# Kernel tuning notes

Measured on AMD Instinct MI355X. Metric: run time of the kernel, lower is better.

## Reference

```python
import jax, jax.numpy as jnp
import numpy as np

DIM = 768
HEADS = 12
HEAD_DIM = DIM // HEADS
SCALE = HEAD_DIM ** -0.5


def setup_inputs() -> dict:
    key = jax.random.key(0)
    k1, k2, k3, k4, k5 = jax.random.split(key, 5)
    B, N, C = 8, 1024, DIM
    x = jax.random.normal(k1, (B, N, C), dtype=jnp.float32)
    scale_emb = jax.random.normal(k2, (1, 1, C), dtype=jnp.float32)
    # nn.Linear weights stored as (out, in); bias only on proj
    w_qkv = jax.random.normal(k3, (3 * C, C), dtype=jnp.float32) * (C ** -0.5)
    w_proj = jax.random.normal(k4, (C, C), dtype=jnp.float32) * (C ** -0.5)
    b_proj = jax.random.normal(k5, (C,), dtype=jnp.float32) * 0.01
    return {"x": x, "scale_emb": scale_emb, "w_qkv": w_qkv, "w_proj": w_proj, "b_proj": b_proj}


def reference(x, scale_emb, w_qkv, w_proj, b_proj):
    B, N, C = x.shape
    H, D = HEADS, HEAD_DIM
    # qkv: (B, N, 3C) -> (3, B, H, N, D)
    qkv = jnp.einsum('bnc,oc->bno', x, w_qkv)
    qkv = qkv.reshape(B, N, 3, H, D).transpose(2, 0, 3, 1, 4)
    q, k, v = qkv[0], qkv[1], qkv[2]
    # scale_emb broadcast to (B, H, N, D) and added to k
    se = jnp.broadcast_to(scale_emb, (B, N, C)).reshape(B, N, H, D).transpose(0, 2, 1, 3)
    k = k + se
    attn_logits = jnp.einsum('bhnd,bhmd->bhnm', q, k) * SCALE
    attn_probs = jax.nn.softmax(attn_logits, axis=-1)
    out = jnp.einsum('bhnm,bhmd->bhnd', attn_probs, v)
    out = out.transpose(0, 2, 1, 3).reshape(B, N, C)
    out = jnp.einsum('bnc,oc->bno', out, w_proj) + b_proj
    return out, attn_probs
```

## Files before the change

kernel.cpp:

```cpp
#include <hip/hip_runtime.h>
#include <hip/hip_bf16.h>


typedef unsigned short u16;
typedef __attribute__((ext_vector_type(8))) short bf16x8;
typedef __attribute__((ext_vector_type(4))) float f32x4;

#define DEVI static __device__ __forceinline__

DEVI u16 f2bf(float f) {
  union { float f; unsigned int u; } v; v.f = f;
  return (u16)((v.u + 0x7fffu + ((v.u >> 16) & 1u)) >> 16);
}

DEVI void gload16(const void* g, void* l) {
  __builtin_amdgcn_global_load_lds(
      (const __attribute__((address_space(1))) unsigned int*)g,
      (__attribute__((address_space(3))) unsigned int*)l, 16, 0, 0);
}

__global__ void cvt_f32_bf16(const float* __restrict__ src, u16* __restrict__ dst, int n4) {
  int i = blockIdx.x * 256 + threadIdx.x;
  if (i >= n4) return;
  float4 f = ((const float4*)src)[i];
  unsigned int lo = f2bf(f.x) | ((unsigned int)f2bf(f.y) << 16);
  unsigned int hi = f2bf(f.z) | ((unsigned int)f2bf(f.w) << 16);
  ((uint2*)dst)[i] = make_uint2(lo, hi);
}

template<int MODE>
__global__ __launch_bounds__(256)
void gemm128(const u16* __restrict__ A, const u16* __restrict__ Bw, int K,
             const float* __restrict__ se,
             u16* __restrict__ qo, u16* __restrict__ ko, u16* __restrict__ vto,
             const float* __restrict__ bias, float* __restrict__ out)
{
  __shared__ u16 lA[128 * 32];
  __shared__ u16 lB[128 * 32];
  const int mt = blockIdx.x, nt = blockIdx.y;
  const int t = threadIdx.x;
  const int w = t >> 6, l = t & 63, lhi = l >> 4, llo = l & 15;
  const int wr = w >> 1, wc = w & 1;

  f32x4 acc[4][4];
#pragma unroll
  for (int m = 0; m < 4; ++m)
#pragma unroll
    for (int n = 0; n < 4; ++n) acc[m][n] = f32x4{0.f, 0.f, 0.f, 0.f};

  const size_t arow0 = (size_t)mt * 128, brow0 = (size_t)nt * 128;

  for (int k0 = 0; k0 < K; k0 += 32) {
#pragma unroll
    for (int r = 0; r < 2; ++r) {
      int idx = r * 256 + t;
      int row = idx >> 2, col = (idx & 3) * 8;
      gload16(A + (arow0 + row) * K + k0 + col, &lA[idx * 8]);
      gload16(Bw + (brow0 + row) * K + k0 + col, &lB[idx * 8]);
    }
    __syncthreads();
    bf16x8 af[4], bfr[4];
#pragma unroll
    for (int m = 0; m < 4; ++m)
      af[m] = *(const bf16x8*)&lA[(wr * 64 + m * 16 + llo) * 32 + lhi * 8];
#pragma unroll
    for (int n = 0; n < 4; ++n)
      bfr[n] = *(const bf16x8*)&lB[(wc * 64 + n * 16 + llo) * 32 + lhi * 8];
#pragma unroll
    for (int m = 0; m < 4; ++m)
#pragma unroll
      for (int n = 0; n < 4; ++n)
        acc[m][n] = __builtin_amdgcn_mfma_f32_16x16x32_bf16(af[m], bfr[n], acc[m][n], 0, 0, 0);
    __syncthreads();
  }

  if (MODE == 0) {
    const int part = nt / 6;
#pragma unroll
    for (int n = 0; n < 4; ++n) {
      const int gcol = (int)brow0 + wc * 64 + n * 16 + llo;
      const int c = gcol - part * 768;
      const int h = c >> 6, d = c & 63;
      const float sev = (part == 1) ? se[c] : 0.f;
#pragma unroll
      for (int m = 0; m < 4; ++m) {
#pragma unroll
        for (int j = 0; j < 4; ++j) {
          const int tok = (int)arow0 + wr * 64 + m * 16 + lhi * 4 + j;
          const int b = tok >> 10, ntok = tok & 1023;
          const size_t bhh = (size_t)(b * 12 + h);
          const float v = acc[m][n][j];
          if (part == 0)      qo[(bhh * 1024 + ntok) * 64 + d] = f2bf(v * 0.125f);
          else if (part == 1) ko[(bhh * 1024 + ntok) * 64 + d] = f2bf(v + sev);
          else                vto[(bhh * 64 + d) * 1024 + ntok] = f2bf(v);
        }
      }
    }
  } else {
#pragma unroll
    for (int m = 0; m < 4; ++m)
#pragma unroll
      for (int j = 0; j < 4; ++j) {
        const int tok = (int)arow0 + wr * 64 + m * 16 + lhi * 4 + j;
#pragma unroll
        for (int n = 0; n < 4; ++n) {
          const int gcol = (int)brow0 + wc * 64 + n * 16 + llo;
          out[(size_t)tok * 768 + gcol] = acc[m][n][j] + bias[gcol];
        }
      }
  }
}

__global__ __launch_bounds__(256)
void attn_fused(const u16* __restrict__ q, const u16* __restrict__ kin,
                const u16* __restrict__ vt, float* __restrict__ probs,
                u16* __restrict__ ao)
{
  __shared__ u16 lq[32 * 64];
  __shared__ u16 lk[256 * 64];
  __shared__ u16 lp[32 * 264];
  __shared__ float red[4][32];
  const int qt = blockIdx.x, bh = blockIdx.y;
  const int t = threadIdx.x;
  const int w = t >> 6, l = t & 63, lhi = l >> 4, llo = l & 15;

  gload16(q + ((size_t)bh * 1024 + qt * 32) * 64 + t * 8, &lq[t * 8]);
  __syncthreads();

  bf16x8 aq[2][2];
#pragma unroll
  for (int m = 0; m < 2; ++m)
#pragma unroll
    for (int kc = 0; kc < 2; ++kc)
      aq[m][kc] = *(const bf16x8*)&lq[(m * 16 + llo) * 64 + kc * 32 + lhi * 8];

  f32x4 acc[4][2][4];
#pragma unroll
  for (int c = 0; c < 4; ++c)
#pragma unroll
    for (int m = 0; m < 2; ++m)
#pragma unroll
      for (int n = 0; n < 4; ++n) acc[c][m][n] = f32x4{0.f, 0.f, 0.f, 0.f};

#pragma unroll
  for (int c = 0; c < 4; ++c) {
    __syncthreads();
#pragma unroll
    for (int r = 0; r < 8; ++r) {
      int idx = r * 256 + t;
      int row = idx >> 3;
      int cb = (idx & 7) * 16;
      bf16x8 val = *(const bf16x8*)(kin + ((size_t)bh * 1024 + c * 256 + row) * 64 + (idx & 7) * 8);
      *(bf16x8*)((char*)lk + row * 128 + (cb ^ ((row & 7) << 4))) = val;
    }
    __syncthreads();
#pragma unroll
    for (int n = 0; n < 4; ++n) {
      const int row = w * 64 + n * 16 + llo;
      const char* rp = (const char*)lk + row * 128;
      const int sw = (row & 7) << 4;
      bf16x8 b0 = *(const bf16x8*)(rp + ((lhi * 16) ^ sw));
      bf16x8 b1 = *(const bf16x8*)(rp + ((64 + lhi * 16) ^ sw));
#pragma unroll
      for (int m = 0; m < 2; ++m) {
        acc[c][m][n] = __builtin_amdgcn_mfma_f32_16x16x32_bf16(aq[m][0], b0, acc[c][m][n], 0, 0, 0);
        acc[c][m][n] = __builtin_amdgcn_mfma_f32_16x16x32_bf16(aq[m][1], b1, acc[c][m][n], 0, 0, 0);
      }
    }
  }

  float rmx[2][4];
#pragma unroll
  for (int m = 0; m < 2; ++m)
#pragma unroll
    for (int j = 0; j < 4; ++j) {
      float v = -1e30f;
#pragma unroll
      for (int c = 0; c < 4; ++c)
#pragma unroll
        for (int n = 0; n < 4; ++n) v = fmaxf(v, acc[c][m][n][j]);
      rmx[m][j] = v;
    }
#pragma unroll
  for (int msk = 1; msk < 16; msk <<= 1)
#pragma unroll
    for (int m = 0; m < 2; ++m)
#pragma unroll
      for (int j = 0; j < 4; ++j)
        rmx[m][j] = fmaxf(rmx[m][j], __shfl_xor(rmx[m][j], msk));
  if (llo == 0) {
#pragma unroll
    for (int m = 0; m < 2; ++m)
#pragma unroll
      for (int j = 0; j < 4; ++j) red[w][m * 16 + lhi * 4 + j] = rmx[m][j];
  }
  __syncthreads();
  float fmx[2][4];
#pragma unroll
  for (int m = 0; m < 2; ++m)
#pragma unroll
    for (int j = 0; j < 4; ++j) {
      int r = m * 16 + lhi * 4 + j;
      fmx[m][j] = fmaxf(fmaxf(red[0][r], red[1][r]), fmaxf(red[2][r], red[3][r]));
    }
  __syncthreads();

  float rsm[2][4];
#pragma unroll
  for (int m = 0; m < 2; ++m)
#pragma unroll
    for (int j = 0; j < 4; ++j) rsm[m][j] = 0.f;
#pragma unroll
  for (int c = 0; c < 4; ++c)
#pragma unroll
    for (int n = 0; n < 4; ++n)
#pragma unroll
      for (int m = 0; m < 2; ++m)
#pragma unroll
        for (int j = 0; j < 4; ++j) {
          float e = __expf(acc[c][m][n][j] - fmx[m][j]);
          acc[c][m][n][j] = e;
          rsm[m][j] += e;
        }
#pragma unroll
  for (int msk = 1; msk < 16; msk <<= 1)
#pragma unroll
    for (int m = 0; m < 2; ++m)
#pragma unroll
      for (int j = 0; j < 4; ++j) rsm[m][j] += __shfl_xor(rsm[m][j], msk);
  if (llo == 0) {
#pragma unroll
    for (int m = 0; m < 2; ++m)
#pragma unroll
      for (int j = 0; j < 4; ++j) red[w][m * 16 + lhi * 4 + j] = rsm[m][j];
  }
  __syncthreads();
  float inv[2][4];
#pragma unroll
  for (int m = 0; m < 2; ++m)
#pragma unroll
    for (int j = 0; j < 4; ++j) {
      int r = m * 16 + lhi * 4 + j;
      inv[m][j] = 1.0f / (red[0][r] + red[1][r] + red[2][r] + red[3][r]);
    }

  const int b = bh / 12, h = bh % 12;
  const u16* vb = vt + (size_t)bh * 65536;
  float* pb = probs + ((size_t)bh * 1024 + qt * 32) * 1024;
  f32x4 acco[2];
  acco[0] = f32x4{0.f, 0.f, 0.f, 0.f};
  acco[1] = f32x4{0.f, 0.f, 0.f, 0.f};

#pragma unroll
  for (int c = 0; c < 4; ++c) {
    __syncthreads();
#pragma unroll
    for (int n = 0; n < 4; ++n) {
      const int kloc = w * 64 + n * 16 + llo;
#pragma unroll
      for (int m = 0; m < 2; ++m)
#pragma unroll
        for (int j = 0; j < 4; ++j) {
          const int r = m * 16 + lhi * 4 + j;
          const float p = acc[c][m][n][j] * inv[m][j];
          pb[(size_t)r * 1024 + c * 256 + kloc] = p;
          lp[r * 264 + kloc] = f2bf(p);
        }
    }
    __syncthreads();
#pragma unroll
    for (int ks = 0; ks < 8; ++ks) {
      bf16x8 a0 = *(const bf16x8*)&lp[llo * 264 + ks * 32 + lhi * 8];
      bf16x8 a1 = *(const bf16x8*)&lp[(16 + llo) * 264 + ks * 32 + lhi * 8];
      bf16x8 v = *(const bf16x8*)(vb + (size_t)(w * 16 + llo) * 1024 + c * 256 + ks * 32 + lhi * 8);
      acco[0] = __builtin_amdgcn_mfma_f32_16x16x32_bf16(a0, v, acco[0], 0, 0, 0);
      acco[1] = __builtin_amdgcn_mfma_f32_16x16x32_bf16(a1, v, acco[1], 0, 0, 0);
    }
  }

#pragma unroll
  for (int m = 0; m < 2; ++m)
#pragma unroll
    for (int j = 0; j < 4; ++j) {
      const int ntok = qt * 32 + m * 16 + lhi * 4 + j;
      const int d = w * 16 + llo;
      ao[((size_t)(b * 1024 + ntok)) * 768 + h * 64 + d] = f2bf(acco[m][j]);
    }
}

extern "C" void kernel_launch(void* const* d_in, const int* in_sizes, int n_in,
                              void* d_out, int out_size, void* d_ws, size_t ws_size,
                              hipStream_t stream) {
  const float* x     = (const float*)d_in[0];
  const float* se    = (const float*)d_in[1];
  const float* wqkv  = (const float*)d_in[2];
  const float* wproj = (const float*)d_in[3];
  const float* bproj = (const float*)d_in[4];
  float* out = (float*)d_out;
  float* probs = out + 6291456;

  if (ws_size < 67633152) return;
  char* ws = (char*)d_ws;
  u16* xb     = (u16*)(ws);
  u16* wqkvb  = (u16*)(ws + 12582912);
  u16* wprojb = (u16*)(ws + 16121856);
  u16* qb     = (u16*)(ws + 17301504);
  u16* kb     = (u16*)(ws + 29884416);
  u16* vtb    = (u16*)(ws + 42467328);
  u16* aob    = (u16*)(ws + 55050240);

  cvt_f32_bf16<<<6144, 256, 0, stream>>>(x, xb, 1572864);
  cvt_f32_bf16<<<1728, 256, 0, stream>>>(wqkv, wqkvb, 442368);
  cvt_f32_bf16<<<576, 256, 0, stream>>>(wproj, wprojb, 147456);
  gemm128<0><<<dim3(64, 18), 256, 0, stream>>>(xb, wqkvb, 768, se, qb, kb, vtb, nullptr, nullptr);
  attn_fused<<<dim3(32, 96), 256, 0, stream>>>(qb, kb, vtb, probs, aob);
  gemm128<1><<<dim3(64, 6), 256, 0, stream>>>(aob, wprojb, 768, nullptr, nullptr, nullptr, nullptr, bproj, out);
}
```

Measured before the change: 724.5 us.

## Rewrite attention as two-pass online softmax with register-only per-wave tiles

Replaces the LDS-staged attention kernel with one where each wave owns 16 query rows and streams K directly from global memory. A first pass computes the running max and sum with online-softmax rescaling, and a second pass recomputes the scores, writes the normalized probabilities and feeds them straight into the PV MFMAs from registers. This removes shared memory, block barriers and the large accumulator array, at the cost of computing QK twice and issuing uncoalesced direct global K and V loads per wave. The K row permutation lets each lane hold 8 contiguous probability columns so it can store them as vector writes.

```diff
diff --git a/kernel.cpp b/kernel.cpp
--- a/kernel.cpp
+++ b/kernel.cpp
@@ -112,180 +112,105 @@
 }
 
 __global__ __launch_bounds__(256)
-void attn_fused(const u16* __restrict__ q, const u16* __restrict__ kin,
-                const u16* __restrict__ vt, float* __restrict__ probs,
-                u16* __restrict__ ao)
+void attn_fused2(const u16* __restrict__ qg, const u16* __restrict__ kg,
+                 const u16* __restrict__ vg, float* __restrict__ probs,
+                 u16* __restrict__ ao)
 {
-  __shared__ u16 lq[32 * 64];
-  __shared__ u16 lk[256 * 64];
-  __shared__ u16 lp[32 * 264];
-  __shared__ float red[4][32];
   const int qt = blockIdx.x, bh = blockIdx.y;
   const int t = threadIdx.x;
   const int w = t >> 6, l = t & 63, lhi = l >> 4, llo = l & 15;
-
-  gload16(q + ((size_t)bh * 1024 + qt * 32) * 64 + t * 8, &lq[t * 8]);
-  __syncthreads();
-
-  bf16x8 aq[2][2];
-#pragma unroll
-  for (int m = 0; m < 2; ++m)
-#pragma unroll
-    for (int kc = 0; kc < 2; ++kc)
-      aq[m][kc] = *(const bf16x8*)&lq[(m * 16 + llo) * 64 + kc * 32 + lhi * 8];
-
-  f32x4 acc[4][2][4];
-#pragma unroll
-  for (int c = 0; c < 4; ++c)
-#pragma unroll
-    for (int m = 0; m < 2; ++m)
-#pragma unroll
-      for (int n = 0; n < 4; ++n) acc[c][m][n] = f32x4{0.f, 0.f, 0.f, 0.f};
-
-#pragma unroll
-  for (int c = 0; c < 4; ++c) {
-    __syncthreads();
-#pragma unroll
-    for (int r = 0; r < 8; ++r) {
-      int idx = r * 256 + t;
-      int row = idx >> 3;
-      int cb = (idx & 7) * 16;
-      bf16x8 val = *(const bf16x8*)(kin + ((size_t)bh * 1024 + c * 256 + row) * 64 + (idx & 7) * 8);
-      *(bf16x8*)((char*)lk + row * 128 + (cb ^ ((row & 7) << 4))) = val;
+  const int q0 = qt * 64 + w * 16;
+
+  const u16* kb = kg + (size_t)bh * 65536;
+  const u16* vb = vg + (size_t)bh * 65536;
+  const u16* qp = qg + ((size_t)bh * 1024 + q0) * 64;
+
+  const bf16x8 qf0 = *(const bf16x8*)(qp + (size_t)llo * 64 + lhi * 8);
+  const bf16x8 qf1 = *(const bf16x8*)(qp + (size_t)llo * 64 + 32 + lhi * 8);
+
+  const int krow = 8 * (llo >> 2) + (llo & 3);
+
+  float m = -1e30f, lsum = 0.f;
+  for (int k0 = 0; k0 < 1024; k0 += 32) {
+    const u16* kp = kb + (size_t)(k0 + krow) * 64 + lhi * 8;
+    bf16x8 k00 = *(const bf16x8*)(kp);
+    bf16x8 k01 = *(const bf16x8*)(kp + 32);
+    bf16x8 k10 = *(const bf16x8*)(kp + 256);
+    bf16x8 k11 = *(const bf16x8*)(kp + 288);
+    f32x4 sA = {0.f, 0.f, 0.f, 0.f}, sB = {0.f, 0.f, 0.f, 0.f};
+    sA = __builtin_amdgcn_mfma_f32_16x16x32_bf16(k00, qf0, sA, 0, 0, 0);
+    sA = __builtin_amdgcn_mfma_f32_16x16x32_bf16(k01, qf1, sA, 0, 0, 0);
+    sB = __builtin_amdgcn_mfma_f32_16x16x32_bf16(k10, qf0, sB, 0, 0, 0);
+    sB = __builtin_amdgcn_mfma_f32_16x16x32_bf16(k11, qf1, sB, 0, 0, 0);
+    float cm = fmaxf(fmaxf(fmaxf(sA[0], sA[1]), fmaxf(sA[2], sA[3])),
+                     fmaxf(fmaxf(sB[0], sB[1]), fmaxf(sB[2], sB[3])));
+    float mn = fmaxf(m, cm);
+    float e = __expf(sA[0] - mn) + __expf(sA[1] - mn) + __expf(sA[2] - mn) +
+              __expf(sA[3] - mn) + __expf(sB[0] - mn) + __expf(sB[1] - mn) +
+              __expf(sB[2] - mn) + __expf(sB[3] - mn);
+    lsum = lsum * __expf(m - mn) + e;
+    m = mn;
+  }
+#pragma unroll
+  for (int msk = 16; msk <= 32; msk <<= 1) {
+    float mo = __shfl_xor(m, msk);
+    float lo = __shfl_xor(lsum, msk);
+    float mn = fmaxf(m, mo);
+    lsum = lsum * __expf(m - mn) + lo * __expf(mo - mn);
+    m = mn;
+  }
+  const float inv = 1.0f / lsum;
+
+  f32x4 o0 = {0.f, 0.f, 0.f, 0.f}, o1 = o0, o2 = o0, o3 = o0;
+  float* pb = probs + ((size_t)bh * 1024 + q0 + llo) * 1024;
+
+  for (int k0 = 0; k0 < 1024; k0 += 32) {
+    const u16* kp = kb + (size_t)(k0 + krow) * 64 + lhi * 8;
+    bf16x8 k00 = *(const bf16x8*)(kp);
+    bf16x8 k01 = *(const bf16x8*)(kp + 32);
+    bf16x8 k10 = *(const bf16x8*)(kp + 256);
+    bf16x8 k11 = *(const bf16x8*)(kp + 288);
+    f32x4 sA = {0.f, 0.f, 0.f, 0.f}, sB = {0.f, 0.f, 0.f, 0.f};
+    sA = __builtin_amdgcn_mfma_f32_16x16x32_bf16(k00, qf0, sA, 0, 0, 0);
+    sA = __builtin_amdgcn_mfma_f32_16x16x32_bf16(k01, qf1, sA, 0, 0, 0);
+    sB = __builtin_amdgcn_mfma_f32_16x16x32_bf16(k10, qf0, sB, 0, 0, 0);
+    sB = __builtin_amdgcn_mfma_f32_16x16x32_bf16(k11, qf1, sB, 0, 0, 0);
+
+    f32x4 pA, pB;
+#pragma unroll
+    for (int j = 0; j < 4; ++j) {
+      pA[j] = __expf(sA[j] - m) * inv;
+      pB[j] = __expf(sB[j] - m) * inv;
     }
-    __syncthreads();
-#pragma unroll
-    for (int n = 0; n < 4; ++n) {
-      const int row = w * 64 + n * 16 + llo;
-      const char* rp = (const char*)lk + row * 128;
-      const int sw = (row & 7) << 4;
-      bf16x8 b0 = *(const bf16x8*)(rp + ((lhi * 16) ^ sw));
-      bf16x8 b1 = *(const bf16x8*)(rp + ((64 + lhi * 16) ^ sw));
-#pragma unroll
-      for (int m = 0; m < 2; ++m) {
-        acc[c][m][n] = __builtin_amdgcn_mfma_f32_16x16x32_bf16(aq[m][0], b0, acc[c][m][n], 0, 0, 0);
-        acc[c][m][n] = __builtin_amdgcn_mfma_f32_16x16x32_bf16(aq[m][1], b1, acc[c][m][n], 0, 0, 0);
-      }
-    }
-  }
-
-  float rmx[2][4];
-#pragma unroll
-  for (int m = 0; m < 2; ++m)
-#pragma unroll
-    for (int j = 0; j < 4; ++j) {
-      float v = -1e30f;
-#pragma unroll
-      for (int c = 0; c < 4; ++c)
-#pragma unroll
-        for (int n = 0; n < 4; ++n) v = fmaxf(v, acc[c][m][n][j]);
-      rmx[m][j] = v;
-    }
-#pragma unroll
-  for (int msk = 1; msk < 16; msk <<= 1)
-#pragma unroll
-    for (int m = 0; m < 2; ++m)
-#pragma unroll
-      for (int j = 0; j < 4; ++j)
-        rmx[m][j] = fmaxf(rmx[m][j], __shfl_xor(rmx[m][j], msk));
-  if (llo == 0) {
-#pragma unroll
-    for (int m = 0; m < 2; ++m)
-#pragma unroll
-      for (int j = 0; j < 4; ++j) red[w][m * 16 + lhi * 4 + j] = rmx[m][j];
-  }
-  __syncthreads();
-  float fmx[2][4];
-#pragma unroll
-  for (int m = 0; m < 2; ++m)
-#pragma unroll
-    for (int j = 0; j < 4; ++j) {
-      int r = m * 16 + lhi * 4 + j;
-      fmx[m][j] = fmaxf(fmaxf(red[0][r], red[1][r]), fmaxf(red[2][r], red[3][r]));
-    }
-  __syncthreads();
-
-  float rsm[2][4];
-#pragma unroll
-  for (int m = 0; m < 2; ++m)
-#pragma unroll
-    for (int j = 0; j < 4; ++j) rsm[m][j] = 0.f;
-#pragma unroll
-  for (int c = 0; c < 4; ++c)
-#pragma unroll
-    for (int n = 0; n < 4; ++n)
-#pragma unroll
-      for (int m = 0; m < 2; ++m)
-#pragma unroll
-        for (int j = 0; j < 4; ++j) {
-          float e = __expf(acc[c][m][n][j] - fmx[m][j]);
-          acc[c][m][n][j] = e;
-          rsm[m][j] += e;
-        }
-#pragma unroll
-  for (int msk = 1; msk < 16; msk <<= 1)
-#pragma unroll
-    for (int m = 0; m < 2; ++m)
-#pragma unroll
-      for (int j = 0; j < 4; ++j) rsm[m][j] += __shfl_xor(rsm[m][j], msk);
-  if (llo == 0) {
-#pragma unroll
-    for (int m = 0; m < 2; ++m)
-#pragma unroll
-      for (int j = 0; j < 4; ++j) red[w][m * 16 + lhi * 4 + j] = rsm[m][j];
-  }
-  __syncthreads();
-  float inv[2][4];
-#pragma unroll
-  for (int m = 0; m < 2; ++m)
-#pragma unroll
-    for (int j = 0; j < 4; ++j) {
-      int r = m * 16 + lhi * 4 + j;
-      inv[m][j] = 1.0f / (red[0][r] + red[1][r] + red[2][r] + red[3][r]);
-    }
+    *(f32x4*)(pb + k0 + lhi * 8) = pA;
+    *(f32x4*)(pb + k0 + lhi * 8 + 4) = pB;
+
+    bf16x8 pa;
+    pa[0] = (short)f2bf(pA[0]); pa[1] = (short)f2bf(pA[1]);
+    pa[2] = (short)f2bf(pA[2]); pa[3] = (short)f2bf(pA[3]);
+    pa[4] = (short)f2bf(pB[0]); pa[5] = (short)f2bf(pB[1]);
+    pa[6] = (short)f2bf(pB[2]); pa[7] = (short)f2bf(pB[3]);
+
+    const u16* vp = vb + (size_t)llo * 1024 + k0 + lhi * 8;
+    bf16x8 v0 = *(const bf16x8*)(vp);
+    bf16x8 v1 = *(const bf16x8*)(vp + 16 * 1024);
+    bf16x8 v2 = *(const bf16x8*)(vp + 32 * 1024);
+    bf16x8 v3 = *(const bf16x8*)(vp + 48 * 1024);
+    o0 = __builtin_amdgcn_mfma_f32_16x16x32_bf16(pa, v0, o0, 0, 0, 0);
+    o1 = __builtin_amdgcn_mfma_f32_16x16x32_bf16(pa, v1, o1, 0, 0, 0);
+    o2 = __builtin_amdgcn_mfma_f32_16x16x32_bf16(pa, v2, o2, 0, 0, 0);
+    o3 = __builtin_amdgcn_mfma_f32_16x16x32_bf16(pa, v3, o3, 0, 0, 0);
+  }
 
   const int b = bh / 12, h = bh % 12;
-  const u16* vb = vt + (size_t)bh * 65536;
-  float* pb = probs + ((size_t)bh * 1024 + qt * 32) * 1024;
-  f32x4 acco[2];
-  acco[0] = f32x4{0.f, 0.f, 0.f, 0.f};
-  acco[1] = f32x4{0.f, 0.f, 0.f, 0.f};
-
-#pragma unroll
-  for (int c = 0; c < 4; ++c) {
-    __syncthreads();
-#pragma unroll
-    for (int n = 0; n < 4; ++n) {
-      const int kloc = w * 64 + n * 16 + llo;
-#pragma unroll
-      for (int m = 0; m < 2; ++m)
-#pragma unroll
-        for (int j = 0; j < 4; ++j) {
-          const int r = m * 16 + lhi * 4 + j;
-          const float p = acc[c][m][n][j] * inv[m][j];
-          pb[(size_t)r * 1024 + c * 256 + kloc] = p;
-          lp[r * 264 + kloc] = f2bf(p);
-        }
-    }
-    __syncthreads();
-#pragma unroll
-    for (int ks = 0; ks < 8; ++ks) {
-      bf16x8 a0 = *(const bf16x8*)&lp[llo * 264 + ks * 32 + lhi * 8];
-      bf16x8 a1 = *(const bf16x8*)&lp[(16 + llo) * 264 + ks * 32 + lhi * 8];
-      bf16x8 v = *(const bf16x8*)(vb + (size_t)(w * 16 + llo) * 1024 + c * 256 + ks * 32 + lhi * 8);
-      acco[0] = __builtin_amdgcn_mfma_f32_16x16x32_bf16(a0, v, acco[0], 0, 0, 0);
-      acco[1] = __builtin_amdgcn_mfma_f32_16x16x32_bf16(a1, v, acco[1], 0, 0, 0);
-    }
-  }
-
-#pragma unroll
-  for (int m = 0; m < 2; ++m)
-#pragma unroll
-    for (int j = 0; j < 4; ++j) {
-      const int ntok = qt * 32 + m * 16 + lhi * 4 + j;
-      const int d = w * 16 + llo;
-      ao[((size_t)(b * 1024 + ntok)) * 768 + h * 64 + d] = f2bf(acco[m][j]);
-    }
+  u16* aop = ao + ((size_t)(b * 1024 + q0 + lhi * 4)) * 768 + h * 64 + llo;
+#pragma unroll
+  for (int j = 0; j < 4; ++j) {
+    aop[(size_t)j * 768 + 0]  = f2bf(o0[j]);
+    aop[(size_t)j * 768 + 16] = f2bf(o1[j]);
+    aop[(size_t)j * 768 + 32] = f2bf(o2[j]);
+    aop[(size_t)j * 768 + 48] = f2bf(o3[j]);
+  }
 }
 
 extern "C" void kernel_launch(void* const* d_in, const int* in_sizes, int n_in,
@@ -313,6 +238,6 @@
   cvt_f32_bf16<<<1728, 256, 0, stream>>>(wqkv, wqkvb, 442368);
   cvt_f32_bf16<<<576, 256, 0, stream>>>(wproj, wprojb, 147456);
   gemm128<0><<<dim3(64, 18), 256, 0, stream>>>(xb, wqkvb, 768, se, qb, kb, vtb, nullptr, nullptr);
-  attn_fused<<<dim3(32, 96), 256, 0, stream>>>(qb, kb, vtb, probs, aob);
+  attn_fused2<<<dim3(16, 96), 256, 0, stream>>>(qb, kb, vtb, probs, aob);
   gemm128<1><<<dim3(64, 6), 256, 0, stream>>>(aob, wprojb, 768, nullptr, nullptr, nullptr, nullptr, bproj, out);
 }
```

Result: slower. 774.9 us (+7.0%).
